# Performance work log

Measured on AMD Instinct MI355X. Metric: run time of the kernel, lower is better.

## Reference

```python
import jax, jax.numpy as jnp
import numpy as np

B, N, F = 8, 2048, 256

def setup_inputs() -> dict:
    key = jax.random.key(0)
    ks = jax.random.split(key, 8)
    X = jax.random.normal(ks[0], (B, N, F), dtype=jnp.float32)
    A_geo = jax.random.uniform(ks[1], (N, N), dtype=jnp.float32)
    distance_matrix = jax.random.uniform(ks[2], (N, N), dtype=jnp.float32)
    W_w = jax.random.normal(ks[3], (F, F), dtype=jnp.float32) * 0.05
    W_b = jax.random.normal(ks[4], (F,), dtype=jnp.float32) * 0.05
    a1 = jax.random.normal(ks[5], (F,), dtype=jnp.float32) * 0.05  # attn_fc weight, first half (for h_i)
    a2 = jax.random.normal(ks[6], (F,), dtype=jnp.float32) * 0.05  # attn_fc weight, second half (for h_j)
    attn_b = jax.random.normal(ks[7], (1,), dtype=jnp.float32) * 0.05
    threshold = jnp.ones((1,), dtype=jnp.float32) * 0.3
    return {"X": X, "A_geo": A_geo, "distance_matrix": distance_matrix,
            "W_w": W_w, "W_b": W_b, "a1": a1, "a2": a2,
            "attn_b": attn_b, "threshold": threshold}

def reference(X, A_geo, distance_matrix, W_w, W_b, a1, a2, attn_b, threshold):
    alpha = 0.1  # leaky relu slope
    h = jnp.einsum('bnf,of->bno', X, W_w) + W_b            # (B,N,F)
    # attn_fc(cat(h_i,h_j)) == h_i@a1 + h_j@a2 + b (linear decomposition of concat)
    s1 = jnp.einsum('bnf,f->bn', h, a1)                    # score contribution of h_i
    s2 = jnp.einsum('bnf,f->bn', h, a2)                    # score contribution of h_j
    e = jax.nn.leaky_relu(s1[:, :, None] + s2[:, None, :] + attn_b[0],
                          negative_slope=alpha)            # (B,N,N)
    n = distance_matrix.shape[0]
    idx = jnp.arange(n)
    D = distance_matrix.at[idx, idx].set(1.0)              # fill_diagonal_(1.0)
    e = e + 1.0 / (D + 1e-5)[None, :, :]
    mask = jax.nn.sigmoid(10.0 * (A_geo - threshold[0]))   # (N,N)
    e = e * mask[None, :, :]
    attention = jax.nn.softmax(e, axis=-1)                 # dropout: eval mode (identity)
    h_prime = jnp.einsum('bnm,bmf->bnf', attention, h)
    return h_prime
```

## Files before the change

### kernel.cpp

```cpp
#include <hip/hip_runtime.h>
#include <hip/hip_bf16.h>
#include <math.h>

#define Bsz 8
#define Nn  2048
#define Ff  256
#define KCAP 1024
#define THR 60.0f

typedef short short8 __attribute__((ext_vector_type(8)));
typedef float f32x4  __attribute__((ext_vector_type(4)));
typedef unsigned short u16x4 __attribute__((ext_vector_type(4)));
typedef unsigned short u16x8 __attribute__((ext_vector_type(8)));
typedef unsigned int uint;

static __device__ __forceinline__ unsigned short f2bf(float v) {
    __hip_bfloat16 b = __float2bfloat16(v);
    return *reinterpret_cast<unsigned short*>(&b);
}
static __device__ __forceinline__ float bf2f(unsigned short u) {
    return __uint_as_float((uint)u << 16);
}
static __device__ __forceinline__ float fast_rcp(float x) {
    return __builtin_amdgcn_rcpf(x);
}

__global__ __launch_bounds__(512) void k_h(const float* __restrict__ X,
                                           const float* __restrict__ W,
                                           const float* __restrict__ Wb,
                                           const float* __restrict__ a1,
                                           const float* __restrict__ a2,
                                           unsigned short* __restrict__ h,
                                           float* __restrict__ s1,
                                           float* __restrict__ s2) {
    __shared__ char smem[45056];
    char* w_lds = smem;
    char* x_lds = smem + 32768;
    float (*sred1)[4][16] = (float(*)[4][16])(smem + 40960);
    float (*sred2)[4][16] = (float(*)[4][16])(smem + 40960 + 2048);

    const int tid  = threadIdx.x;
    const int lane = tid & 63;
    const int w    = tid >> 6;
    const int r0   = blockIdx.x * 64;
    const int b    = r0 >> 11;
    const int n0   = r0 & 2047;

    f32x4 acc[2][4];
#pragma unroll
    for (int mt = 0; mt < 2; mt++)
#pragma unroll
        for (int nt = 0; nt < 4; nt++) acc[mt][nt] = (f32x4)0.f;

    float4 wv[8], xv[2];
    auto gload = [&](int kc) {
        const int f0 = kc * 64;
#pragma unroll
        for (int p = 0; p < 8; p++) {
            int idx = tid + p * 512;
            int o = idx >> 4, fi = idx & 15;
            wv[p] = *(const float4*)&W[(size_t)o * Ff + f0 + fi * 4];
        }
#pragma unroll
        for (int p = 0; p < 2; p++) {
            int idx = tid + p * 512;
            int n = idx >> 4, fi = idx & 15;
            xv[p] = *(const float4*)&X[(size_t)(r0 + n) * Ff + f0 + fi * 4];
        }
    };
    auto swrite = [&]() {
#pragma unroll
        for (int p = 0; p < 8; p++) {
            int idx = tid + p * 512;
            int o = idx >> 4, fi = idx & 15;
            u16x4 pk = {f2bf(wv[p].x), f2bf(wv[p].y), f2bf(wv[p].z), f2bf(wv[p].w)};
            *(u16x4*)(w_lds + ((o * 128 + fi * 8) ^ ((o & 7) << 4))) = pk;
        }
#pragma unroll
        for (int p = 0; p < 2; p++) {
            int idx = tid + p * 512;
            int n = idx >> 4, fi = idx & 15;
            u16x4 pk = {f2bf(xv[p].x), f2bf(xv[p].y), f2bf(xv[p].z), f2bf(xv[p].w)};
            *(u16x4*)(x_lds + ((n * 128 + fi * 8) ^ ((n & 7) << 4))) = pk;
        }
    };

    gload(0);
    for (int kc = 0; kc < 4; kc++) {
        __syncthreads();
        swrite();
        __syncthreads();
        if (kc < 3) gload(kc + 1);
#pragma unroll
        for (int kt = 0; kt < 2; kt++) {
            short8 bfr[4];
#pragma unroll
            for (int nt = 0; nt < 4; nt++) {
                int n = nt * 16 + (lane & 15);
                bfr[nt] = *(const short8*)(x_lds + ((n * 128 + kt * 64 + (lane >> 4) * 16) ^ ((n & 7) << 4)));
            }
#pragma unroll
            for (int mt = 0; mt < 2; mt++) {
                int o = w * 32 + mt * 16 + (lane & 15);
                short8 afr = *(const short8*)(w_lds + ((o * 128 + kt * 64 + (lane >> 4) * 16) ^ ((o & 7) << 4)));
#pragma unroll
                for (int nt = 0; nt < 4; nt++)
                    acc[mt][nt] = __builtin_amdgcn_mfma_f32_16x16x32_bf16(afr, bfr[nt], acc[mt][nt], 0, 0, 0);
            }
        }
    }

    __syncthreads();
    float s1p[4] = {0.f, 0.f, 0.f, 0.f};
    float s2p[4] = {0.f, 0.f, 0.f, 0.f};
#pragma unroll
    for (int mt = 0; mt < 2; mt++) {
#pragma unroll
        for (int reg = 0; reg < 4; reg++) {
            int o = w * 32 + mt * 16 + (lane >> 4) * 4 + reg;
            float wb = Wb[o], a1v = a1[o], a2v = a2[o];
#pragma unroll
            for (int nt = 0; nt < 4; nt++) {
                float hv = acc[mt][nt][reg] + wb;
                int nl = nt * 16 + (lane & 15);
                *(unsigned short*)(w_lds + nl * 512 + ((o * 2) ^ ((nl & 7) << 4))) = f2bf(hv);
                s1p[nt] += hv * a1v;
                s2p[nt] += hv * a2v;
            }
        }
    }
#pragma unroll
    for (int nt = 0; nt < 4; nt++) {
        s1p[nt] += __shfl_xor(s1p[nt], 16); s1p[nt] += __shfl_xor(s1p[nt], 32);
        s2p[nt] += __shfl_xor(s2p[nt], 16); s2p[nt] += __shfl_xor(s2p[nt], 32);
    }
    if (lane < 16) {
#pragma unroll
        for (int nt = 0; nt < 4; nt++) { sred1[w][nt][lane] = s1p[nt]; sred2[w][nt][lane] = s2p[nt]; }
    }
    __syncthreads();

#pragma unroll
    for (int p = 0; p < 4; p++) {
        int id = tid + p * 512;
        int nl = id >> 5;
        int c16 = (id & 31) * 16;
        u16x8 v = *(const u16x8*)(w_lds + nl * 512 + (c16 ^ ((nl & 7) << 4)));
        *(u16x8*)&h[((size_t)(b * Nn + n0 + nl)) * Ff + (id & 31) * 8] = v;
    }
    if (tid < 64) {
        int nt = tid >> 4, col = tid & 15;
        float v = 0.f;
#pragma unroll
        for (int k = 0; k < 8; k++) v += sred1[k][nt][col];
        s1[b * Nn + n0 + nt * 16 + col] = v;
    } else if (tid < 128) {
        int t2 = tid - 64;
        int nt = t2 >> 4, col = t2 & 15;
        float v = 0.f;
#pragma unroll
        for (int k = 0; k < 8; k++) v += sred2[k][nt][col];
        s2[b * Nn + n0 + nt * 16 + col] = v;
    }
}

__global__ __launch_bounds__(256) void k_attn(const unsigned short* __restrict__ h,
                                              const float* __restrict__ s1,
                                              const float* __restrict__ s2,
                                              const float* __restrict__ Ageo,
                                              const float* __restrict__ Dm,
                                              const float* __restrict__ ab_p,
                                              const float* __restrict__ thr_p,
                                              float* __restrict__ out) {
    __shared__ uint  ejs[KCAP];
    __shared__ float emks[KCAP];
    __shared__ float edgs[KCAP];
    __shared__ float red[4];
    __shared__ uint  cptr;

    const int i    = blockIdx.x;
    const int tid  = threadIdx.x;
    const int lane = tid & 63;
    const int w    = tid >> 6;
    const float c10 = 10.0f * thr_p[0];

    const int b0 = w, b1 = w + 4;
    const float ab = ab_p[0];
    const float s1v0 = s1[b0 * Nn + i] + ab;
    const float s1v1 = s1[b1 * Nn + i] + ab;
    const float* s2b0 = s2 + b0 * Nn;
    const float* s2b1 = s2 + b1 * Nn;
    const unsigned short* h0 = h + (size_t)b0 * Nn * Ff;
    const unsigned short* h1 = h + (size_t)b1 * Nn * Ff;

    if (tid == 0) cptr = 0;
    const int j0 = tid * 8;
    float4 a0 = *(const float4*)&Ageo[(size_t)i * Nn + j0];
    float4 a1v = *(const float4*)&Ageo[(size_t)i * Nn + j0 + 4];
    float4 d0 = *(const float4*)&Dm[(size_t)i * Nn + j0];
    float4 d1 = *(const float4*)&Dm[(size_t)i * Nn + j0 + 4];
    float av[8] = {a0.x, a0.y, a0.z, a0.w, a1v.x, a1v.y, a1v.z, a1v.w};
    float dv[8] = {d0.x, d0.y, d0.z, d0.w, d1.x, d1.y, d1.z, d1.w};
    float mk[8], gg[8];
    float m = 0.0f;
#pragma unroll
    for (int c = 0; c < 8; c++) {
        float dd = (j0 + c == i) ? 1.0f : dv[c];
        float mkv = fast_rcp(1.0f + __expf(c10 - 10.0f * av[c]));
        float g   = mkv * fast_rcp(dd + 1e-5f);
        mk[c] = mkv;
        gg[c] = g;
        m = fmaxf(m, g);
    }
#pragma unroll
    for (int dd = 32; dd; dd >>= 1) m = fmaxf(m, __shfl_xor(m, dd));
    if (lane == 0) red[w] = m;
    __syncthreads();
    float gmax = fmaxf(fmaxf(red[0], red[1]), fmaxf(red[2], red[3]));
    const float cut = gmax - THR;
#pragma unroll
    for (int c = 0; c < 8; c++) {
        if (gg[c] > cut) {
            uint slot = atomicAdd(&cptr, 1u);
            if (slot < KCAP) {
                ejs[slot]  = (uint)(j0 + c);
                emks[slot] = mk[c];
                edgs[slot] = gg[c] - gmax;
            }
        }
    }
    __syncthreads();
    const int C = min(cptr, (uint)KCAP);

    float4 acc0 = make_float4(0.f, 0.f, 0.f, 0.f);
    float4 acc1 = make_float4(0.f, 0.f, 0.f, 0.f);
    float ps0 = 0.f, ps1 = 0.f;

    uint  jA  = ejs[0];
    float mkA = emks[0];
    float dgA = edgs[0];
    float s2A0 = s2b0[jA], s2A1 = s2b1[jA];
    ushort4 hvA0 = *(const ushort4*)&h0[(size_t)jA * Ff + lane * 4];
    ushort4 hvA1 = *(const ushort4*)&h1[(size_t)jA * Ff + lane * 4];

    for (int c = 0; c < C; c++) {
        int cn = (c + 1 < C) ? c + 1 : c;
        uint  jB  = ejs[cn];
        float mkB = emks[cn];
        float dgB = edgs[cn];
        float s2B0 = s2b0[jB], s2B1 = s2b1[jB];
        ushort4 hvB0 = *(const ushort4*)&h0[(size_t)jB * Ff + lane * 4];
        ushort4 hvB1 = *(const ushort4*)&h1[(size_t)jB * Ff + lane * 4];

        float sa = s1v0 + s2A0;
        sa = sa > 0.f ? sa : 0.1f * sa;
        float p0 = __expf(sa * mkA + dgA);
        ps0 += p0;
        acc0.x += p0 * bf2f(hvA0.x);
        acc0.y += p0 * bf2f(hvA0.y);
        acc0.z += p0 * bf2f(hvA0.z);
        acc0.w += p0 * bf2f(hvA0.w);

        float sb = s1v1 + s2A1;
        sb = sb > 0.f ? sb : 0.1f * sb;
        float p1 = __expf(sb * mkA + dgA);
        ps1 += p1;
        acc1.x += p1 * bf2f(hvA1.x);
        acc1.y += p1 * bf2f(hvA1.y);
        acc1.z += p1 * bf2f(hvA1.z);
        acc1.w += p1 * bf2f(hvA1.w);

        jA = jB; mkA = mkB; dgA = dgB;
        s2A0 = s2B0; s2A1 = s2B1; hvA0 = hvB0; hvA1 = hvB1;
    }

    float inv0 = 1.0f / ps0;
    float inv1 = 1.0f / ps1;
    *(float4*)&out[((size_t)(b0 * Nn + i)) * Ff + lane * 4] =
        make_float4(acc0.x * inv0, acc0.y * inv0, acc0.z * inv0, acc0.w * inv0);
    *(float4*)&out[((size_t)(b1 * Nn + i)) * Ff + lane * 4] =
        make_float4(acc1.x * inv1, acc1.y * inv1, acc1.z * inv1, acc1.w * inv1);
}

extern "C" void kernel_launch(void* const* d_in, const int* in_sizes, int n_in,
                              void* d_out, int out_size, void* d_ws, size_t ws_size,
                              hipStream_t stream) {
    const float* X    = (const float*)d_in[0];
    const float* Ageo = (const float*)d_in[1];
    const float* Dm   = (const float*)d_in[2];
    const float* Ww   = (const float*)d_in[3];
    const float* Wb   = (const float*)d_in[4];
    const float* a1   = (const float*)d_in[5];
    const float* a2   = (const float*)d_in[6];
    const float* ab   = (const float*)d_in[7];
    const float* thr  = (const float*)d_in[8];
    float* out = (float*)d_out;

    char* ws = (char*)d_ws;
    float* s1 = (float*)ws;
    float* s2 = s1 + (size_t)Bsz * Nn;
    unsigned short* h = (unsigned short*)(s2 + (size_t)Bsz * Nn);

    k_h<<<256, 512, 0, stream>>>(X, Ww, Wb, a1, a2, h, s1, s2);
    k_attn<<<Nn, 256, 0, stream>>>(h, s1, s2, Ageo, Dm, ab, thr, out);
}
```

Before: 27.26 us.

## Load W fragments directly into registers and stage full X tile once

The projection kernel no longer stages W through LDS across four k-chunks with paired barriers. Each wave now loads its own W rows straight from global memory into bf16 MFMA fragments held in registers, and the whole 64x256 X tile is converted and written to LDS once behind a single barrier. This removes the per-chunk barriers and the LDS round-trip for W. In exchange it raises register pressure (64 short8 fragments per lane), uses less coalesced strided W loads, and drops the overlap of loads with compute.

```diff
diff --git a/kernel.cpp b/kernel.cpp
--- a/kernel.cpp
+++ b/kernel.cpp
@@ -33,11 +33,10 @@
                                            unsigned short* __restrict__ h,
                                            float* __restrict__ s1,
                                            float* __restrict__ s2) {
-    __shared__ char smem[45056];
-    char* w_lds = smem;
-    char* x_lds = smem + 32768;
-    float (*sred1)[4][16] = (float(*)[4][16])(smem + 40960);
-    float (*sred2)[4][16] = (float(*)[4][16])(smem + 40960 + 2048);
+    __shared__ char smem[36864];
+    char* x_lds = smem;
+    float (*sred1)[4][16] = (float(*)[4][16])(smem + 32768);
+    float (*sred2)[4][16] = (float(*)[4][16])(smem + 32768 + 2048);
 
     const int tid  = threadIdx.x;
     const int lane = tid & 63;
@@ -46,67 +45,64 @@
     const int b    = r0 >> 11;
     const int n0   = r0 & 2047;
 
+    float4 xv[8];
+#pragma unroll
+    for (int p = 0; p < 8; p++) {
+        int idx = tid + p * 512;
+        int n = idx >> 6, fi = idx & 63;
+        xv[p] = *(const float4*)&X[(size_t)(r0 + n) * Ff + fi * 4];
+    }
+
+    short8 wfrag[2][4][2];
+#pragma unroll
+    for (int mt = 0; mt < 2; mt++) {
+        const int o = w * 32 + mt * 16 + (lane & 15);
+        const float* wrow = W + (size_t)o * Ff + (lane >> 4) * 8;
+#pragma unroll
+        for (int kc = 0; kc < 4; kc++)
+#pragma unroll
+            for (int kt = 0; kt < 2; kt++) {
+                float4 lo = *(const float4*)(wrow + kc * 64 + kt * 32);
+                float4 hi = *(const float4*)(wrow + kc * 64 + kt * 32 + 4);
+                short8 f;
+                f[0] = (short)f2bf(lo.x); f[1] = (short)f2bf(lo.y);
+                f[2] = (short)f2bf(lo.z); f[3] = (short)f2bf(lo.w);
+                f[4] = (short)f2bf(hi.x); f[5] = (short)f2bf(hi.y);
+                f[6] = (short)f2bf(hi.z); f[7] = (short)f2bf(hi.w);
+                wfrag[mt][kc][kt] = f;
+            }
+    }
+
+#pragma unroll
+    for (int p = 0; p < 8; p++) {
+        int idx = tid + p * 512;
+        int n = idx >> 6, fi = idx & 63;
+        u16x4 pk = {f2bf(xv[p].x), f2bf(xv[p].y), f2bf(xv[p].z), f2bf(xv[p].w)};
+        *(u16x4*)(x_lds + ((n * 512 + fi * 8) ^ ((n & 7) << 4))) = pk;
+    }
+    __syncthreads();
+
     f32x4 acc[2][4];
 #pragma unroll
     for (int mt = 0; mt < 2; mt++)
 #pragma unroll
         for (int nt = 0; nt < 4; nt++) acc[mt][nt] = (f32x4)0.f;
 
-    float4 wv[8], xv[2];
-    auto gload = [&](int kc) {
-        const int f0 = kc * 64;
-#pragma unroll
-        for (int p = 0; p < 8; p++) {
-            int idx = tid + p * 512;
-            int o = idx >> 4, fi = idx & 15;
-            wv[p] = *(const float4*)&W[(size_t)o * Ff + f0 + fi * 4];
-        }
-#pragma unroll
-        for (int p = 0; p < 2; p++) {
-            int idx = tid + p * 512;
-            int n = idx >> 4, fi = idx & 15;
-            xv[p] = *(const float4*)&X[(size_t)(r0 + n) * Ff + f0 + fi * 4];
-        }
-    };
-    auto swrite = [&]() {
-#pragma unroll
-        for (int p = 0; p < 8; p++) {
-            int idx = tid + p * 512;
-            int o = idx >> 4, fi = idx & 15;
-            u16x4 pk = {f2bf(wv[p].x), f2bf(wv[p].y), f2bf(wv[p].z), f2bf(wv[p].w)};
-            *(u16x4*)(w_lds + ((o * 128 + fi * 8) ^ ((o & 7) << 4))) = pk;
-        }
-#pragma unroll
-        for (int p = 0; p < 2; p++) {
-            int idx = tid + p * 512;
-            int n = idx >> 4, fi = idx & 15;
-            u16x4 pk = {f2bf(xv[p].x), f2bf(xv[p].y), f2bf(xv[p].z), f2bf(xv[p].w)};
-            *(u16x4*)(x_lds + ((n * 128 + fi * 8) ^ ((n & 7) << 4))) = pk;
-        }
-    };
-
-    gload(0);
+#pragma unroll
     for (int kc = 0; kc < 4; kc++) {
-        __syncthreads();
-        swrite();
-        __syncthreads();
-        if (kc < 3) gload(kc + 1);
 #pragma unroll
         for (int kt = 0; kt < 2; kt++) {
             short8 bfr[4];
 #pragma unroll
             for (int nt = 0; nt < 4; nt++) {
                 int n = nt * 16 + (lane & 15);
-                bfr[nt] = *(const short8*)(x_lds + ((n * 128 + kt * 64 + (lane >> 4) * 16) ^ ((n & 7) << 4)));
+                bfr[nt] = *(const short8*)(x_lds + ((n * 512 + kc * 128 + kt * 64 + (lane >> 4) * 16) ^ ((n & 7) << 4)));
             }
 #pragma unroll
-            for (int mt = 0; mt < 2; mt++) {
-                int o = w * 32 + mt * 16 + (lane & 15);
-                short8 afr = *(const short8*)(w_lds + ((o * 128 + kt * 64 + (lane >> 4) * 16) ^ ((o & 7) << 4)));
+            for (int mt = 0; mt < 2; mt++)
 #pragma unroll
                 for (int nt = 0; nt < 4; nt++)
-                    acc[mt][nt] = __builtin_amdgcn_mfma_f32_16x16x32_bf16(afr, bfr[nt], acc[mt][nt], 0, 0, 0);
-            }
+                    acc[mt][nt] = __builtin_amdgcn_mfma_f32_16x16x32_bf16(wfrag[mt][kc][kt], bfr[nt], acc[mt][nt], 0, 0, 0);
         }
     }
 
@@ -123,7 +119,7 @@
             for (int nt = 0; nt < 4; nt++) {
                 float hv = acc[mt][nt][reg] + wb;
                 int nl = nt * 16 + (lane & 15);
-                *(unsigned short*)(w_lds + nl * 512 + ((o * 2) ^ ((nl & 7) << 4))) = f2bf(hv);
+                *(unsigned short*)(x_lds + nl * 512 + ((o * 2) ^ ((nl & 7) << 4))) = f2bf(hv);
                 s1p[nt] += hv * a1v;
                 s2p[nt] += hv * a2v;
             }
@@ -145,7 +141,7 @@
         int id = tid + p * 512;
         int nl = id >> 5;
         int c16 = (id & 31) * 16;
-        u16x8 v = *(const u16x8*)(w_lds + nl * 512 + (c16 ^ ((nl & 7) << 4)));
+        u16x8 v = *(const u16x8*)(x_lds + nl * 512 + (c16 ^ ((nl & 7) << 4)));
         *(u16x8*)&h[((size_t)(b * Nn + n0 + nl)) * Ff + (id & 31) * 8] = v;
     }
     if (tid < 64) {
```

Result: slower. 31.32 us (+14.9%).
